# Optimization experiments

Measured on AMD Instinct MI355X. Metric: run time of the kernel, lower is better.

## Reference

```python
import jax, jax.numpy as jnp
import numpy as np

RX = 2  # matches init rx
RY = 2  # matches init ry


def _bilinear_gather(img, coords):
    """Bilinear sample with zero padding (mirrors grid_sample align_corners=True, padding_mode='zeros').
    img: [C,H,W]; coords: [P,2] pixel-space (x,y). Returns [C,P]."""
    C, H, W = img.shape
    x, y = coords[:, 0], coords[:, 1]
    x0, y0 = jnp.floor(x), jnp.floor(y)
    wx, wy = x - x0, y - y0

    def tap(xi, yi, w):
        valid = (xi >= 0) & (xi <= W - 1) & (yi >= 0) & (yi <= H - 1)
        xc = jnp.clip(xi, 0, W - 1).astype(jnp.int32)
        yc = jnp.clip(yi, 0, H - 1).astype(jnp.int32)
        v = img[:, yc, xc]  # [C,P] gather
        return v * (w * valid.astype(w.dtype))[None, :]

    return (tap(x0, y0, (1 - wx) * (1 - wy)) + tap(x0 + 1, y0, wx * (1 - wy))
            + tap(x0, y0 + 1, (1 - wx) * wy) + tap(x0 + 1, y0 + 1, wx * wy))


def _local_cost_volume(flow, f1, f2, rx, ry):
    """build_sample_cv: windowed bilinear gather of f2 around (grid + flow), dot with f1.
    Returns cv [N,H,W,2ry+1,2rx+1] with window ordered (dy,dx)."""
    N, C, H, W = f1.shape
    dt = f1.dtype
    gy, gx = jnp.meshgrid(jnp.arange(H, dtype=dt), jnp.arange(W, dtype=dt), indexing='ij')
    base = jnp.stack([gx, gy], 0)[None]            # [1,2,H,W] (x,y) like coords_grid
    cen = (base + flow).transpose(0, 2, 3, 1)       # [N,H,W,2]
    dx = jnp.linspace(-rx, rx, 2 * rx + 1).astype(dt)
    dy = jnp.linspace(-ry, ry, 2 * ry + 1).astype(dt)
    mgy, mgx = jnp.meshgrid(dy, dx, indexing='ij')  # [dH,dW]
    off = jnp.stack([mgx, mgy], -1)                 # [dH,dW,2] (x,y)
    dH, dW = 2 * ry + 1, 2 * rx + 1
    coords = cen[:, None, None] + off[None, :, :, None, None, :]  # [N,dH,dW,H,W,2]
    coords = coords.reshape(N, dH * dW * H * W, 2)
    samp = jax.vmap(_bilinear_gather)(f2, coords)   # [N,C,dH*dW*H*W]
    samp = samp.reshape(N, C, dH, dW, H, W)
    # cv[n,h,w,i,j] = sum_c f1[n,c,h,w] * f2_sampled[n,c,i,j,h,w]
    cv = jnp.einsum('nchw,ncijhw->nhwij', f1, samp)
    return cv


def setup_inputs() -> dict:
    key = jax.random.key(0)
    k1, k2, k3 = jax.random.split(key, 3)
    N, C, H, W = 2, 256, 55, 128
    return {
        'flow': jax.random.normal(k1, (N, 2, H, W), dtype=jnp.float32),
        'f1': jax.random.normal(k2, (N, C, H, W), dtype=jnp.float32),
        'f2': jax.random.normal(k3, (N, C, H, W), dtype=jnp.float32),
    }


def reference(flow, f1, f2):
    cv = _local_cost_volume(flow, f1, f2, RX, RY)   # [N,H,W,dH,dW]
    N, H, W, dH, dW = cv.shape
    flat = cv.reshape(N, H, W, dH * dW)
    # WTA over the last two (window) dims, as in get_argmax_NHW_xy_last_th
    wta_val = jnp.max(flat, axis=-1)
    idx = jnp.argmax(flat, axis=-1)
    wta_xy = jnp.stack([idx % dW, idx // dW], axis=0)  # [2,N,H,W] (x,y)
    return cv, wta_val, wta_xy
```

## Files before the change

### kernel.cpp

```cpp
#include <hip/hip_runtime.h>

#define N_   2
#define C_   256
#define H_   55
#define W_   128
#define HW_  (H_ * W_)
#define NPIX (N_ * HW_)
#define PB   16
#define PW   4
#define NBLK (NPIX / PB)
#define BPX  (NBLK / 8)
#define F1LD 260

#define OFF_CV  0
#define OFF_VAL (NPIX * 25)
#define OFF_XY  (OFF_VAL + NPIX)

__global__ __launch_bounds__(256) void transpose_f2(const float* __restrict__ f2,
                                                    float* __restrict__ f2t) {
    __shared__ float tile[64][65];
    const int n = blockIdx.z;
    const float* __restrict__ src = f2 + (size_t)n * C_ * HW_;
    float* __restrict__ dst = f2t + (size_t)n * HW_ * C_;

    const int p0 = blockIdx.x * 64;
    const int c0 = blockIdx.y * 64;
    const int q = threadIdx.x & 15;
    const int r = threadIdx.x >> 4;

    #pragma unroll
    for (int rr = r; rr < 64; rr += 16) {
        const float4 v = *(const float4*)(src + (size_t)(c0 + rr) * HW_ + p0 + q * 4);
        tile[rr][q * 4 + 0] = v.x;
        tile[rr][q * 4 + 1] = v.y;
        tile[rr][q * 4 + 2] = v.z;
        tile[rr][q * 4 + 3] = v.w;
    }
    __syncthreads();

    #pragma unroll
    for (int j = 0; j < 4; ++j) {
        const int pr = r + 16 * j;
        float4 v;
        v.x = tile[q * 4 + 0][pr];
        v.y = tile[q * 4 + 1][pr];
        v.z = tile[q * 4 + 2][pr];
        v.w = tile[q * 4 + 3][pr];
        *(float4*)(dst + (size_t)(p0 + pr) * C_ + c0 + q * 4) = v;
    }
}

__device__ __forceinline__ float dot4(const float4 a, const float4 b) {
    return a.x * b.x + a.y * b.y + a.z * b.z + a.w * b.w;
}

__global__ __launch_bounds__(256) void costvol_kernel(const float* __restrict__ flow,
                                                      const float* __restrict__ f1,
                                                      const float* __restrict__ f2t,
                                                      float* __restrict__ out) {
    __shared__ float f1sh[PB][F1LD];
    __shared__ float Dsh[4][36];

    const int b    = blockIdx.x;
    const int xcd  = b & 7;
    const int kk   = b >> 3;
    const int pix0 = (xcd * BPX + kk) * PB;
    const int n     = pix0 / HW_;
    const int prem0 = pix0 - n * HW_;
    const int h     = prem0 >> 7;
    const int w0    = prem0 & (W_ - 1);

    {
        const int px4   = threadIdx.x & 3;
        const int cbase = threadIdx.x >> 2;
        #pragma unroll
        for (int it = 0; it < 4; ++it) {
            const int c = cbase + it * 64;
            const float4 v = *(const float4*)(f1 + ((size_t)n * C_ + c) * HW_ + prem0 + px4 * 4);
            f1sh[px4 * 4 + 0][c] = v.x;
            f1sh[px4 * 4 + 1][c] = v.y;
            f1sh[px4 * 4 + 2][c] = v.z;
            f1sh[px4 * 4 + 3][c] = v.w;
        }
    }
    __syncthreads();

    const int wv   = threadIdx.x >> 6;
    const int lane = threadIdx.x & 63;
    const int sgrp = lane >> 4;
    const int cgrp = lane & 15;

    const float4* __restrict__ f2base = (const float4*)(f2t + (size_t)n * HW_ * C_);
    const float* __restrict__ flown   = flow + (size_t)n * 2 * HW_;

    for (int pp = 0; pp < PW; ++pp) {
        const int pl  = wv * PW + pp;
        const int pix = pix0 + pl;
        const int w   = w0 + pl;

        const float fx = flown[h * W_ + w];
        const float fy = flown[HW_ + h * W_ + w];
        const float cx = (float)w + fx;
        const float cy = (float)h + fy;
        const float x0f = floorf(cx), y0f = floorf(cy);
        const float wx = cx - x0f, wy = cy - y0f;
        const int ix0 = (int)x0f, iy0 = (int)y0f;

        const float* fr = &f1sh[pl][cgrp * 4];
        const float4 a0 = *(const float4*)(fr);
        const float4 a1 = *(const float4*)(fr + 64);
        const float4 a2 = *(const float4*)(fr + 128);
        const float4 a3 = *(const float4*)(fr + 192);

        #pragma unroll
        for (int p = 0; p < 9; ++p) {
            const int s  = p * 4 + sgrp;
            const int ly = s / 6, lx = s - ly * 6;
            const int sy = iy0 - 2 + ly;
            const int sx = ix0 - 2 + lx;
            float part = 0.f;
            if (sy >= 0 && sy < H_ && sx >= 0 && sx < W_) {
                const float4* __restrict__ bp =
                    f2base + (size_t)(sy * W_ + sx) * (C_ / 4) + cgrp;
                part = dot4(a0, bp[0]) + dot4(a1, bp[16])
                     + dot4(a2, bp[32]) + dot4(a3, bp[48]);
            }
            part += __shfl_xor(part, 1, 64);
            part += __shfl_xor(part, 2, 64);
            part += __shfl_xor(part, 4, 64);
            part += __shfl_xor(part, 8, 64);
            if (cgrp == 0) Dsh[wv][s] = part;
        }
        __builtin_amdgcn_wave_barrier();

        float cv = 0.f;
        if (lane < 25) {
            const int i = lane / 5, j = lane - i * 5;
            const float D00 = Dsh[wv][i * 6 + j];
            const float D01 = Dsh[wv][i * 6 + j + 1];
            const float D10 = Dsh[wv][i * 6 + j + 6];
            const float D11 = Dsh[wv][i * 6 + j + 7];
            cv = (1.f - wx) * (1.f - wy) * D00 + wx * (1.f - wy) * D01
               + (1.f - wx) * wy * D10 + wx * wy * D11;
            out[OFF_CV + (size_t)pix * 25 + lane] = cv;
        }

        float v  = (lane < 25) ? cv : -3.4e38f;
        int  idx = (lane < 25) ? lane : 25;
        #pragma unroll
        for (int off = 16; off >= 1; off >>= 1) {
            const float v2 = __shfl_down(v, off, 32);
            const int   i2 = __shfl_down(idx, off, 32);
            if (v2 > v || (v2 == v && i2 < idx)) { v = v2; idx = i2; }
        }
        if (lane == 0) {
            out[OFF_VAL + pix] = v;
            out[OFF_XY + pix]        = (float)(idx % 5);
            out[OFF_XY + NPIX + pix] = (float)(idx / 5);
        }
        __builtin_amdgcn_wave_barrier();
    }
}

extern "C" void kernel_launch(void* const* d_in, const int* in_sizes, int n_in,
                              void* d_out, int out_size, void* d_ws, size_t ws_size,
                              hipStream_t stream) {
    const float* flow = (const float*)d_in[0];
    const float* f1   = (const float*)d_in[1];
    const float* f2   = (const float*)d_in[2];
    float* out = (float*)d_out;

    float* f2t = (float*)d_ws;

    transpose_f2<<<dim3(HW_ / 64, C_ / 64, N_), 256, 0, stream>>>(f2, f2t);
    costvol_kernel<<<dim3(NBLK), 256, 0, stream>>>(flow, f1, f2t, out);
}
```

Before: 103.5 us.

## Prefetch f2 window taps with clamped loads and use DPP row reductions

The 9 per-lane window loads now use clamped addresses and are issued unconditionally, two iterations ahead through a three-slot register buffer. Validity is applied after the dot product, and the cross-lane sums are batched at the end using DPP row operations instead of shuffles. This aims to hide gather latency and cut the cost of the shuffle reductions. It raises register pressure, which launch_bounds(256,4) constrains.

```diff
diff --git a/kernel.cpp b/kernel.cpp
--- a/kernel.cpp
+++ b/kernel.cpp
@@ -54,10 +54,23 @@
     return a.x * b.x + a.y * b.y + a.z * b.z + a.w * b.w;
 }
 
-__global__ __launch_bounds__(256) void costvol_kernel(const float* __restrict__ flow,
-                                                      const float* __restrict__ f1,
-                                                      const float* __restrict__ f2t,
-                                                      float* __restrict__ out) {
+__device__ __forceinline__ float dpp_add16(float x) {
+    int v;
+    v = __builtin_amdgcn_update_dpp(0, __float_as_int(x), 0xB1, 0xF, 0xF, true);
+    x += __int_as_float(v);
+    v = __builtin_amdgcn_update_dpp(0, __float_as_int(x), 0x4E, 0xF, 0xF, true);
+    x += __int_as_float(v);
+    v = __builtin_amdgcn_update_dpp(0, __float_as_int(x), 0x141, 0xF, 0xF, true);
+    x += __int_as_float(v);
+    v = __builtin_amdgcn_update_dpp(0, __float_as_int(x), 0x140, 0xF, 0xF, true);
+    x += __int_as_float(v);
+    return x;
+}
+
+__global__ __launch_bounds__(256, 4) void costvol_kernel(const float* __restrict__ flow,
+                                                         const float* __restrict__ f1,
+                                                         const float* __restrict__ f2t,
+                                                         float* __restrict__ out) {
     __shared__ float f1sh[PB][F1LD];
     __shared__ float Dsh[4][36];
 
@@ -90,6 +103,14 @@
     const int sgrp = lane >> 4;
     const int cgrp = lane & 15;
 
+    int lyv[9], lxv[9];
+    #pragma unroll
+    for (int p = 0; p < 9; ++p) {
+        const int s = p * 4 + sgrp;
+        lyv[p] = s / 6;
+        lxv[p] = s - 6 * lyv[p];
+    }
+
     const float4* __restrict__ f2base = (const float4*)(f2t + (size_t)n * HW_ * C_);
     const float* __restrict__ flown   = flow + (size_t)n * 2 * HW_;
 
@@ -112,24 +133,38 @@
         const float4 a2 = *(const float4*)(fr + 128);
         const float4 a3 = *(const float4*)(fr + 192);
 
+        float4 bbs[3][4];
+        float  D[9];
+
+#define ISSUE(p, slot) {                                                        \
+            const int sy = iy0 - 2 + lyv[p];                                    \
+            const int sx = ix0 - 2 + lxv[p];                                    \
+            const int scy = min(max(sy, 0), H_ - 1);                            \
+            const int scx = min(max(sx, 0), W_ - 1);                            \
+            const float4* __restrict__ bp =                                     \
+                f2base + (size_t)(scy * W_ + scx) * (C_ / 4) + cgrp;            \
+            bbs[slot][0] = bp[0];  bbs[slot][1] = bp[16];                       \
+            bbs[slot][2] = bp[32]; bbs[slot][3] = bp[48]; }
+
+        ISSUE(0, 0)
+        ISSUE(1, 1)
         #pragma unroll
         for (int p = 0; p < 9; ++p) {
-            const int s  = p * 4 + sgrp;
-            const int ly = s / 6, lx = s - ly * 6;
-            const int sy = iy0 - 2 + ly;
-            const int sx = ix0 - 2 + lx;
-            float part = 0.f;
-            if (sy >= 0 && sy < H_ && sx >= 0 && sx < W_) {
-                const float4* __restrict__ bp =
-                    f2base + (size_t)(sy * W_ + sx) * (C_ / 4) + cgrp;
-                part = dot4(a0, bp[0]) + dot4(a1, bp[16])
-                     + dot4(a2, bp[32]) + dot4(a3, bp[48]);
-            }
-            part += __shfl_xor(part, 1, 64);
-            part += __shfl_xor(part, 2, 64);
-            part += __shfl_xor(part, 4, 64);
-            part += __shfl_xor(part, 8, 64);
-            if (cgrp == 0) Dsh[wv][s] = part;
+            if (p < 7) ISSUE(p + 2, (p + 2) % 3)
+            const int slot = p % 3;
+            const int sy = iy0 - 2 + lyv[p];
+            const int sx = ix0 - 2 + lxv[p];
+            const bool vld = ((unsigned)sy < (unsigned)H_) && ((unsigned)sx < (unsigned)W_);
+            const float part = dot4(a0, bbs[slot][0]) + dot4(a1, bbs[slot][1])
+                             + dot4(a2, bbs[slot][2]) + dot4(a3, bbs[slot][3]);
+            D[p] = vld ? part : 0.f;
+        }
+#undef ISSUE
+
+        #pragma unroll
+        for (int p = 0; p < 9; ++p) {
+            const float t = dpp_add16(D[p]);
+            if (cgrp == 0) Dsh[wv][p * 4 + sgrp] = t;
         }
         __builtin_amdgcn_wave_barrier();
 
```

Measured after the change: 176.0 us. 70.0% more time.

## Stage shared f2 window region in LDS per block with 512 threads

Applied to the files above, without the earlier changes.

Each block now computes the bounding box of the sampled f2 neighbourhoods for its 16 pixels. When that box fits in 12 rows by 32 columns, it stages the f2 tile into LDS in channel chunks, and each wave accumulates dot products for two pixels from shared memory. The goal is to stop repeatedly fetching overlapping f2 rows from global/L2. If the box is too large, the block falls back to the direct-gather path. The change also doubles the block size to 512, replaces shuffle reductions with DPP adds, and uses nontemporal loads and stores. The cost is many more __syncthreads per block (16 in the chunk loop) and a large LDS footprint. With random unit-normal flow the rows usually span about 8 to 10, so the staged path should mostly be taken.

```diff
diff --git a/kernel.cpp b/kernel.cpp
--- a/kernel.cpp
+++ b/kernel.cpp
@@ -7,14 +7,19 @@
 #define HW_  (H_ * W_)
 #define NPIX (N_ * HW_)
 #define PB   16
-#define PW   4
 #define NBLK (NPIX / PB)
 #define BPX  (NBLK / 8)
 #define F1LD 260
+#define MAXR 12
+#define NCOL 32
+#define SLOTS (MAXR * NCOL)
+#define SLD  36
 
 #define OFF_CV  0
 #define OFF_VAL (NPIX * 25)
 #define OFF_XY  (OFF_VAL + NPIX)
+
+typedef float f32x4 __attribute__((ext_vector_type(4)));
 
 __global__ __launch_bounds__(256) void transpose_f2(const float* __restrict__ f2,
                                                     float* __restrict__ f2t) {
@@ -30,7 +35,8 @@
 
     #pragma unroll
     for (int rr = r; rr < 64; rr += 16) {
-        const float4 v = *(const float4*)(src + (size_t)(c0 + rr) * HW_ + p0 + q * 4);
+        const f32x4 v = __builtin_nontemporal_load(
+            (const f32x4*)(src + (size_t)(c0 + rr) * HW_ + p0 + q * 4));
         tile[rr][q * 4 + 0] = v.x;
         tile[rr][q * 4 + 1] = v.y;
         tile[rr][q * 4 + 2] = v.z;
@@ -54,13 +60,70 @@
     return a.x * b.x + a.y * b.y + a.z * b.z + a.w * b.w;
 }
 
-__global__ __launch_bounds__(256) void costvol_kernel(const float* __restrict__ flow,
-                                                      const float* __restrict__ f1,
-                                                      const float* __restrict__ f2t,
-                                                      float* __restrict__ out) {
-    __shared__ float f1sh[PB][F1LD];
-    __shared__ float Dsh[4][36];
-
+__device__ __forceinline__ float dpp_add16(float x) {
+    int v;
+    v = __builtin_amdgcn_update_dpp(0, __float_as_int(x), 0xB1, 0xF, 0xF, true);
+    x += __int_as_float(v);
+    v = __builtin_amdgcn_update_dpp(0, __float_as_int(x), 0x4E, 0xF, 0xF, true);
+    x += __int_as_float(v);
+    v = __builtin_amdgcn_update_dpp(0, __float_as_int(x), 0x141, 0xF, 0xF, true);
+    x += __int_as_float(v);
+    v = __builtin_amdgcn_update_dpp(0, __float_as_int(x), 0x140, 0xF, 0xF, true);
+    x += __int_as_float(v);
+    return x;
+}
+
+__device__ __forceinline__ float dpp_add8(float x) {
+    int v;
+    v = __builtin_amdgcn_update_dpp(0, __float_as_int(x), 0xB1, 0xF, 0xF, true);
+    x += __int_as_float(v);
+    v = __builtin_amdgcn_update_dpp(0, __float_as_int(x), 0x4E, 0xF, 0xF, true);
+    x += __int_as_float(v);
+    v = __builtin_amdgcn_update_dpp(0, __float_as_int(x), 0x141, 0xF, 0xF, true);
+    x += __int_as_float(v);
+    return x;
+}
+
+__device__ __forceinline__ void blend_wta(const float* __restrict__ Drow,
+                                          float wx, float wy, int pix, int lane,
+                                          float* __restrict__ out) {
+    float cv = 0.f;
+    if (lane < 25) {
+        const int i = lane / 5, j = lane - i * 5;
+        const float D00 = Drow[i * 6 + j];
+        const float D01 = Drow[i * 6 + j + 1];
+        const float D10 = Drow[i * 6 + j + 6];
+        const float D11 = Drow[i * 6 + j + 7];
+        cv = (1.f - wx) * (1.f - wy) * D00 + wx * (1.f - wy) * D01
+           + (1.f - wx) * wy * D10 + wx * wy * D11;
+        __builtin_nontemporal_store(cv, out + OFF_CV + (size_t)pix * 25 + lane);
+    }
+    float v  = (lane < 25) ? cv : -3.4e38f;
+    int  idx = (lane < 25) ? lane : 25;
+    #pragma unroll
+    for (int off = 16; off >= 1; off >>= 1) {
+        const float v2 = __shfl_down(v, off, 32);
+        const int   i2 = __shfl_down(idx, off, 32);
+        if (v2 > v || (v2 == v && i2 < idx)) { v = v2; idx = i2; }
+    }
+    if (lane == 0) {
+        __builtin_nontemporal_store(v, out + OFF_VAL + pix);
+        __builtin_nontemporal_store((float)(idx % 5), out + OFF_XY + pix);
+        __builtin_nontemporal_store((float)(idx / 5), out + OFF_XY + NPIX + pix);
+    }
+}
+
+__global__ __launch_bounds__(512, 4) void costvol_kernel(const float* __restrict__ flow,
+                                                         const float* __restrict__ f1,
+                                                         const float* __restrict__ f2t,
+                                                         float* __restrict__ out) {
+    __shared__ __align__(16) float f1sh[PB][F1LD];
+    __shared__ __align__(16) float stage[SLOTS * SLD];
+    __shared__ float Dsh[8][36];
+    __shared__ float wxs[PB], wys[PB];
+    __shared__ int   ix0s[PB], iy0s[PB];
+
+    const int tid  = threadIdx.x;
     const int b    = blockIdx.x;
     const int xcd  = b & 7;
     const int kk   = b >> 3;
@@ -70,13 +133,25 @@
     const int h     = prem0 >> 7;
     const int w0    = prem0 & (W_ - 1);
 
+    const float* __restrict__ flown = flow + (size_t)n * 2 * HW_;
+    if (tid < PB) {
+        const float fx = flown[h * W_ + w0 + tid];
+        const float fy = flown[HW_ + h * W_ + w0 + tid];
+        const float cx = (float)(w0 + tid) + fx;
+        const float cy = (float)h + fy;
+        const float x0f = floorf(cx), y0f = floorf(cy);
+        wxs[tid] = cx - x0f;  wys[tid] = cy - y0f;
+        ix0s[tid] = (int)x0f; iy0s[tid] = (int)y0f;
+    }
+
     {
-        const int px4   = threadIdx.x & 3;
-        const int cbase = threadIdx.x >> 2;
+        const int px4   = tid & 3;
+        const int cbase = tid >> 2;
         #pragma unroll
-        for (int it = 0; it < 4; ++it) {
-            const int c = cbase + it * 64;
-            const float4 v = *(const float4*)(f1 + ((size_t)n * C_ + c) * HW_ + prem0 + px4 * 4);
+        for (int it = 0; it < 2; ++it) {
+            const int c = cbase + it * 128;
+            const f32x4 v = __builtin_nontemporal_load(
+                (const f32x4*)(f1 + ((size_t)n * C_ + c) * HW_ + prem0 + px4 * 4));
             f1sh[px4 * 4 + 0][c] = v.x;
             f1sh[px4 * 4 + 1][c] = v.y;
             f1sh[px4 * 4 + 2][c] = v.z;
@@ -85,80 +160,106 @@
     }
     __syncthreads();
 
-    const int wv   = threadIdx.x >> 6;
-    const int lane = threadIdx.x & 63;
-    const int sgrp = lane >> 4;
-    const int cgrp = lane & 15;
-
-    const float4* __restrict__ f2base = (const float4*)(f2t + (size_t)n * HW_ * C_);
-    const float* __restrict__ flown   = flow + (size_t)n * 2 * HW_;
-
-    for (int pp = 0; pp < PW; ++pp) {
-        const int pl  = wv * PW + pp;
-        const int pix = pix0 + pl;
-        const int w   = w0 + pl;
-
-        const float fx = flown[h * W_ + w];
-        const float fy = flown[HW_ + h * W_ + w];
-        const float cx = (float)w + fx;
-        const float cy = (float)h + fy;
-        const float x0f = floorf(cx), y0f = floorf(cy);
-        const float wx = cx - x0f, wy = cy - y0f;
-        const int ix0 = (int)x0f, iy0 = (int)y0f;
-
-        const float* fr = &f1sh[pl][cgrp * 4];
-        const float4 a0 = *(const float4*)(fr);
-        const float4 a1 = *(const float4*)(fr + 64);
-        const float4 a2 = *(const float4*)(fr + 128);
-        const float4 a3 = *(const float4*)(fr + 192);
-
-        #pragma unroll
-        for (int p = 0; p < 9; ++p) {
-            const int s  = p * 4 + sgrp;
-            const int ly = s / 6, lx = s - ly * 6;
-            const int sy = iy0 - 2 + ly;
-            const int sx = ix0 - 2 + lx;
-            float part = 0.f;
-            if (sy >= 0 && sy < H_ && sx >= 0 && sx < W_) {
-                const float4* __restrict__ bp =
-                    f2base + (size_t)(sy * W_ + sx) * (C_ / 4) + cgrp;
-                part = dot4(a0, bp[0]) + dot4(a1, bp[16])
-                     + dot4(a2, bp[32]) + dot4(a3, bp[48]);
+    int mnIx = ix0s[0], mxIx = ix0s[0], mnIy = iy0s[0], mxIy = iy0s[0];
+    #pragma unroll
+    for (int t = 1; t < PB; ++t) {
+        mnIx = min(mnIx, ix0s[t]); mxIx = max(mxIx, ix0s[t]);
+        mnIy = min(mnIy, iy0s[t]); mxIy = max(mxIy, iy0s[t]);
+    }
+    const int Ra  = max(mnIy - 2, 0);
+    const int Rb  = min(mxIy + 3, H_ - 1);
+    const int NRc = Rb - Ra + 1;
+    const int Xb  = min(max(mnIx - 2, 0) & ~3, W_ - NCOL);
+    const bool fb = (NRc < 1) || (NRc > MAXR) ||
+                    ((min(mxIx + 3, W_ - 1) - Xb) > NCOL - 1);
+    const int fbu = __builtin_amdgcn_readfirstlane((int)fb);
+
+    const int wv   = tid >> 6;
+    const int lane = tid & 63;
+    const float4* __restrict__ f2t4 = (const float4*)f2t + (size_t)n * HW_ * (C_ / 4);
+
+    if (!fbu) {
+        const int oct = lane >> 3;
+        const int cg  = lane & 7;
+        float4* __restrict__ st4 = (float4*)stage;
+        const float4* __restrict__ f1sh4 = (const float4*)&f1sh[0][0];
+        const int plA = wv * 2, plB = wv * 2 + 1;
+        const int ix0A = ix0s[plA], iy0A = iy0s[plA];
+        const int ix0B = ix0s[plB], iy0B = iy0s[plB];
+
+#define SPRE(S, P)                                                              \
+        int slot##S##P; float msk##S##P; float D##S##P = 0.f;                   \
+        { const int s  = (P) * 8 + oct;                                         \
+          const int dy = s / 6;                                                 \
+          const int sy = iy0##S - 2 + dy, sx = ix0##S - 2 + (s - 6 * dy);       \
+          const bool vv = (s < 36) && ((unsigned)sy < (unsigned)H_) &&          \
+                          ((unsigned)sx < (unsigned)W_);                        \
+          slot##S##P = vv ? ((sy - Ra) * NCOL + (sx - Xb)) : 0;                 \
+          msk##S##P  = vv ? 1.f : 0.f; }
+        SPRE(A,0) SPRE(A,1) SPRE(A,2) SPRE(A,3) SPRE(A,4)
+        SPRE(B,0) SPRE(B,1) SPRE(B,2) SPRE(B,3) SPRE(B,4)
+#undef SPRE
+
+        const int nf4 = NRc * 256;
+        for (int k = 0; k < 8; ++k) {
+            for (int j = tid; j < nf4; j += 512) {
+                const int q = j & 7, slot = j >> 3;
+                const int col = slot & (NCOL - 1), rr = slot >> 5;
+                st4[slot * (SLD / 4) + q] =
+                    f2t4[(size_t)((Ra + rr) * W_ + Xb + col) * (C_ / 4) + k * 8 + q];
             }
-            part += __shfl_xor(part, 1, 64);
-            part += __shfl_xor(part, 2, 64);
-            part += __shfl_xor(part, 4, 64);
-            part += __shfl_xor(part, 8, 64);
-            if (cgrp == 0) Dsh[wv][s] = part;
+            __syncthreads();
+            const float4 aA = f1sh4[plA * (F1LD / 4) + k * 8 + cg];
+            const float4 aB = f1sh4[plB * (F1LD / 4) + k * 8 + cg];
+#define SACC(S, P) { const float4 vq = st4[slot##S##P * (SLD / 4) + cg];        \
+                     D##S##P += msk##S##P * dot4(a##S, vq); }
+            SACC(A,0) SACC(A,1) SACC(A,2) SACC(A,3) SACC(A,4)
+            SACC(B,0) SACC(B,1) SACC(B,2) SACC(B,3) SACC(B,4)
+#undef SACC
+            __syncthreads();
         }
+
+#define SRED(S, P) { const float t = dpp_add8(D##S##P);                         \
+                     const int s = (P) * 8 + oct;                               \
+                     if (cg == 0 && s < 36) Dsh[wv][s] = t; }
+        SRED(A,0) SRED(A,1) SRED(A,2) SRED(A,3) SRED(A,4)
         __builtin_amdgcn_wave_barrier();
-
-        float cv = 0.f;
-        if (lane < 25) {
-            const int i = lane / 5, j = lane - i * 5;
-            const float D00 = Dsh[wv][i * 6 + j];
-            const float D01 = Dsh[wv][i * 6 + j + 1];
-            const float D10 = Dsh[wv][i * 6 + j + 6];
-            const float D11 = Dsh[wv][i * 6 + j + 7];
-            cv = (1.f - wx) * (1.f - wy) * D00 + wx * (1.f - wy) * D01
-               + (1.f - wx) * wy * D10 + wx * wy * D11;
-            out[OFF_CV + (size_t)pix * 25 + lane] = cv;
+        blend_wta(Dsh[wv], wxs[plA], wys[plA], pix0 + plA, lane, out);
+        __builtin_amdgcn_wave_barrier();
+        SRED(B,0) SRED(B,1) SRED(B,2) SRED(B,3) SRED(B,4)
+        __builtin_amdgcn_wave_barrier();
+        blend_wta(Dsh[wv], wxs[plB], wys[plB], pix0 + plB, lane, out);
+#undef SRED
+    } else {
+        const int sgrp = lane >> 4;
+        const int cgrp = lane & 15;
+        for (int pp = 0; pp < 2; ++pp) {
+            const int pl  = wv * 2 + pp;
+            const int ix0 = ix0s[pl], iy0 = iy0s[pl];
+            const float* fr = &f1sh[pl][cgrp * 4];
+            const float4 a0 = *(const float4*)(fr);
+            const float4 a1 = *(const float4*)(fr + 64);
+            const float4 a2 = *(const float4*)(fr + 128);
+            const float4 a3 = *(const float4*)(fr + 192);
+            #pragma unroll
+            for (int p = 0; p < 9; ++p) {
+                const int s  = p * 4 + sgrp;
+                const int ly = s / 6, lx = s - 6 * ly;
+                const int sy = iy0 - 2 + ly, sx = ix0 - 2 + lx;
+                float part = 0.f;
+                if (((unsigned)sy < (unsigned)H_) && ((unsigned)sx < (unsigned)W_)) {
+                    const float4* __restrict__ bp =
+                        f2t4 + (size_t)(sy * W_ + sx) * (C_ / 4) + cgrp;
+                    part = dot4(a0, bp[0]) + dot4(a1, bp[16])
+                         + dot4(a2, bp[32]) + dot4(a3, bp[48]);
+                }
+                part = dpp_add16(part);
+                if (cgrp == 0) Dsh[wv][s] = part;
+            }
+            __builtin_amdgcn_wave_barrier();
+            blend_wta(Dsh[wv], wxs[pl], wys[pl], pix0 + pl, lane, out);
+            __builtin_amdgcn_wave_barrier();
         }
-
-        float v  = (lane < 25) ? cv : -3.4e38f;
-        int  idx = (lane < 25) ? lane : 25;
-        #pragma unroll
-        for (int off = 16; off >= 1; off >>= 1) {
-            const float v2 = __shfl_down(v, off, 32);
-            const int   i2 = __shfl_down(idx, off, 32);
-            if (v2 > v || (v2 == v && i2 < idx)) { v = v2; idx = i2; }
-        }
-        if (lane == 0) {
-            out[OFF_VAL + pix] = v;
-            out[OFF_XY + pix]        = (float)(idx % 5);
-            out[OFF_XY + NPIX + pix] = (float)(idx / 5);
-        }
-        __builtin_amdgcn_wave_barrier();
     }
 }
 
@@ -173,5 +274,5 @@
     float* f2t = (float*)d_ws;
 
     transpose_f2<<<dim3(HW_ / 64, C_ / 64, N_), 256, 0, stream>>>(f2, f2t);
-    costvol_kernel<<<dim3(NBLK), 256, 0, stream>>>(flow, f1, f2t, out);
-}
+    costvol_kernel<<<dim3(NBLK), 512, 0, stream>>>(flow, f1, f2t, out);
+}
```

After: 294.0 us. 2.84x slower.
